# Performance work log

Hardware: AMD Instinct MI355X
Metric: run time of the kernel (lower is better)

## Reference

```python
import jax, jax.numpy as jnp
import numpy as np

N_NODES = 50000
N_EDGES = 800000
HIDDEN = 128
HEADS = 4
HEAD_DIM = HIDDEN // HEADS
LAYERS = 2


def _lin(k, fan_in, fan_out):
    # xavier_uniform with gain=0.1, stored as [in, out]
    lim = 0.1 * np.sqrt(6.0 / (fan_in + fan_out))
    return jax.random.uniform(k, (fan_in, fan_out), jnp.float32, -lim, lim)


def setup_inputs() -> dict:
    key = jax.random.key(0)
    ks = jax.random.split(key, 20)
    x = jax.random.normal(ks[0], (N_NODES, HIDDEN), jnp.float32)
    edge_index = jax.random.randint(ks[1], (2, N_EDGES), 0, N_NODES, jnp.int64)
    Wi = _lin(ks[2], HIDDEN, HIDDEN); bi = jnp.zeros((HIDDEN,), jnp.float32)
    def stack(base):
        kk = jax.random.split(jax.random.fold_in(key, base), LAYERS)
        return jnp.stack([_lin(kk[l], HIDDEN, HIDDEN) for l in range(LAYERS)])
    Wq, Wk, Wv, Wo = stack(10), stack(11), stack(12), stack(13)
    bq = jnp.zeros((LAYERS, HIDDEN), jnp.float32)
    bk = jnp.zeros((LAYERS, HIDDEN), jnp.float32)
    bv = jnp.zeros((LAYERS, HIDDEN), jnp.float32)
    bo = jnp.zeros((LAYERS, HIDDEN), jnp.float32)
    kk1 = jax.random.split(jax.random.fold_in(key, 20), LAYERS)
    kk2 = jax.random.split(jax.random.fold_in(key, 21), LAYERS)
    W1 = jnp.stack([_lin(kk1[l], HIDDEN, 2 * HIDDEN) for l in range(LAYERS)])
    b1 = jnp.zeros((LAYERS, 2 * HIDDEN), jnp.float32)
    W2 = jnp.stack([_lin(kk2[l], 2 * HIDDEN, HIDDEN) for l in range(LAYERS)])
    b2 = jnp.zeros((LAYERS, HIDDEN), jnp.float32)
    return {"x": x, "edge_index": edge_index, "Wi": Wi, "bi": bi,
            "Wq": Wq, "bq": bq, "Wk": Wk, "bk": bk, "Wv": Wv, "bv": bv,
            "Wo": Wo, "bo": bo, "W1": W1, "b1": b1, "W2": W2, "b2": b2}


def _layer(x, src, dst, Wq, bq, Wk, bk, Wv, bv, Wo, bo, W1, b1, W2, b2):
    n = x.shape[0]
    residual = x
    q = (x @ Wq + bq).reshape(n, HEADS, HEAD_DIM)
    k = (x @ Wk + bk).reshape(n, HEADS, HEAD_DIM)
    v = (x @ Wv + bv).reshape(n, HEADS, HEAD_DIM)
    q_i = q[dst]            # [E, H, D]
    k_j = k[src]            # [E, H, D]
    scale = HEAD_DIM ** -0.5
    scores = jnp.einsum('ehd,ehd->eh', q_i, k_j) * scale  # [E, H]
    # NOTE: faithful to original — softmax over ALL edges (dim=0), per head
    attn = jax.nn.softmax(scores, axis=0)
    attn_out = v[src] * attn[:, :, None]  # [E, H, D]
    agg = jax.ops.segment_sum(attn_out, dst, num_segments=n)  # [N, H, D]
    out = agg.reshape(n, HIDDEN) @ Wo + bo
    x = residual + out
    residual = x
    x = jax.nn.relu(x @ W1 + b1) @ W2 + b2
    return residual + x


def reference(x, edge_index, Wi, bi, Wq, bq, Wk, bk, Wv, bv, Wo, bo, W1, b1, W2, b2):
    src, dst = edge_index[0], edge_index[1]
    x = x @ Wi + bi
    for l in range(LAYERS):
        x = _layer(x, src, dst, Wq[l], bq[l], Wk[l], bk[l], Wv[l], bv[l],
                   Wo[l], bo[l], W1[l], b1[l], W2[l], b2[l])
    return x
```

## Files before the change

### kernel.cpp

```cpp
#include <hip/hip_runtime.h>


typedef __attribute__((ext_vector_type(8))) short bf16x8;
typedef __attribute__((ext_vector_type(4))) float f32x4;

__device__ __forceinline__ unsigned short f2bf_rne(float f) {
  unsigned int u = __builtin_bit_cast(unsigned int, f);
  u = (u + 0x7fffu + ((u >> 16) & 1u)) >> 16;
  return (unsigned short)u;
}
__device__ __forceinline__ unsigned int pack2bf(float a, float b) {
  return (unsigned int)f2bf_rne(a) | ((unsigned int)f2bf_rne(b) << 16);
}
__device__ __forceinline__ float bflo(unsigned int w) {
  return __builtin_bit_cast(float, w << 16);
}
__device__ __forceinline__ float bfhi(unsigned int w) {
  return __builtin_bit_cast(float, w & 0xffff0000u);
}

template<bool RELU, bool RES, bool OUTF, bool OUTB, bool QKVH, bool AF32>
__global__ __launch_bounds__(256)
void mgemm_k(const void* __restrict__ Ain,
             const unsigned short* __restrict__ Bt,
             const float* __restrict__ bias, const float* __restrict__ R,
             float* __restrict__ Yf, unsigned short* __restrict__ Yb,
             int M, int K, int N) {
  __shared__ __align__(16) char smem[32768];
  const int t = threadIdx.x;
  const int l = t & 63;
  const int w = t >> 6, wm = w >> 1, wn = w & 1;
  const int row0 = blockIdx.x * 64;
  const int col0 = blockIdx.y * 64;

  f32x4 acc[2][2];
#pragma unroll
  for (int m = 0; m < 2; m++)
#pragma unroll
    for (int n = 0; n < 2; n++)
#pragma unroll
      for (int r = 0; r < 4; r++) acc[m][n][r] = 0.f;

  for (int kc = 0; kc < K; kc += 128) {
    if (kc) __syncthreads();
#pragma unroll
    for (int j = 0; j < 4; j++) {
      int id = j * 256 + t;
      int row = id >> 4, c16 = id & 15;
      int gr = row0 + row; if (gr >= M) gr = M - 1;
      uint4 val;
      if (AF32) {
        const float* ap = (const float*)Ain + (size_t)gr * K + kc + c16 * 8;
        float4 f0 = *(const float4*)ap;
        float4 f1 = *(const float4*)(ap + 4);
        val.x = pack2bf(f0.x, f0.y); val.y = pack2bf(f0.z, f0.w);
        val.z = pack2bf(f1.x, f1.y); val.w = pack2bf(f1.z, f1.w);
      } else {
        val = *(const uint4*)((const unsigned short*)Ain + (size_t)gr * K + kc + c16 * 8);
      }
      *(uint4*)(smem + row * 256 + ((c16 * 16) ^ ((row & 7) << 4))) = val;
    }
#pragma unroll
    for (int j = 0; j < 4; j++) {
      int id = j * 256 + t;
      int row = id >> 4, c16 = id & 15;
      uint4 val = *(const uint4*)(Bt + (size_t)(col0 + row) * K + kc + c16 * 8);
      *(uint4*)(smem + 16384 + row * 256 + ((c16 * 16) ^ ((row & 7) << 4))) = val;
    }
    __syncthreads();

#pragma unroll
    for (int ks = 0; ks < 4; ks++) {
      const int bofs = ks * 64 + (l >> 4) * 16;
      bf16x8 a[2], b[2];
#pragma unroll
      for (int m = 0; m < 2; m++) {
        int r = wm * 32 + m * 16 + (l & 15);
        a[m] = *(const bf16x8*)(smem + r * 256 + (bofs ^ ((r & 7) << 4)));
      }
#pragma unroll
      for (int n = 0; n < 2; n++) {
        int r = wn * 32 + n * 16 + (l & 15);
        b[n] = *(const bf16x8*)(smem + 16384 + r * 256 + (bofs ^ ((r & 7) << 4)));
      }
#pragma unroll
      for (int m = 0; m < 2; m++)
#pragma unroll
        for (int n = 0; n < 2; n++)
          acc[m][n] = __builtin_amdgcn_mfma_f32_16x16x32_bf16(a[m], b[n], acc[m][n], 0, 0, 0);
    }
  }

  const int rbase = row0 + wm * 32 + ((l >> 4) << 2);
  const int cl = l & 15;
#pragma unroll
  for (int n = 0; n < 2; n++) {
    int col = col0 + wn * 32 + n * 16 + cl;
    float bb = bias[col];
#pragma unroll
    for (int m = 0; m < 2; m++) {
      int rtile = rbase + m * 16;
#pragma unroll
      for (int r = 0; r < 4; r++) {
        int row = rtile + r;
        if (row < M) {
          float o = acc[m][n][r] + bb;
          if (RES) o += R[(size_t)row * N + col];
          if (RELU) o = fmaxf(o, 0.f);
          if (OUTF) Yf[(size_t)row * N + col] = o;
          if (OUTB) {
            unsigned short vb = f2bf_rne(o);
            if (QKVH) {
              if (col < 128) {
                Yb[(size_t)row * 128 + col] = vb;
              } else if (col < 256) {
                int cc = col - 128, head = cc >> 5, dd = cc & 31;
                Yb[(size_t)M * 128 + ((size_t)head * M + row) * 32 + dd] = vb;
              } else {
                Yb[(size_t)M * 256 + (size_t)row * 128 + (col - 256)] = vb;
              }
            } else {
              Yb[(size_t)row * N + col] = vb;
            }
          }
        }
      }
    }
  }
}

__global__ __launch_bounds__(256)
void wtc_k(const float* __restrict__ src, unsigned short* __restrict__ dst,
           int K, int N, int cnt, int dstStrideM) {
  int o = blockIdx.x * 256 + threadIdx.x;
  int total = cnt * K * N;
  if (o >= total) return;
  int m = o / (K * N);
  int rem = o - m * K * N;
  int n = rem / K;
  int k = rem - n * K;
  dst[(size_t)m * dstStrideM + (size_t)n * K + k] = f2bf_rne(src[(size_t)m * K * N + (size_t)k * N + n]);
}

__global__ __launch_bounds__(256)
void bcat_k(const float* __restrict__ bq, const float* __restrict__ bk,
            const float* __restrict__ bv, float* __restrict__ bqkv) {
  int idx = blockIdx.x * 256 + threadIdx.x;
  if (idx >= 768) return;
  int l = idx / 384, c = idx - l * 384;
  float v = (c < 128) ? bq[l * 128 + c] : (c < 256) ? bk[l * 128 + c - 128] : bv[l * 128 + c - 256];
  bqkv[idx] = v;
}

__global__ __launch_bounds__(256)
void rs_hist8_k(const int* __restrict__ key, int* __restrict__ gh,
                int E, int shift, int nblk) {
  __shared__ int h[256];
  int t = threadIdx.x, b = blockIdx.x;
  h[t] = 0;
  __syncthreads();
#pragma unroll
  for (int j = 0; j < 8; j++) {
    int i = b * 2048 + j * 256 + t;
    if (i < E) atomicAdd(&h[(key[i] >> shift) & 255], 1);
  }
  __syncthreads();
  gh[t * nblk + b] = h[t];
}

__global__ __launch_bounds__(256)
void scanA_k(const int* __restrict__ a, int* __restrict__ bsum, int n) {
  __shared__ int sm[256];
  int b = blockIdx.x, t = threadIdx.x;
  int base = b * 2048 + t * 8;
  int s = 0;
#pragma unroll
  for (int j = 0; j < 8; j++) {
    int i = base + j;
    if (i < n) s += a[i];
  }
  sm[t] = s; __syncthreads();
  for (int d = 128; d >= 1; d >>= 1) {
    if (t < d) sm[t] += sm[t + d];
    __syncthreads();
  }
  if (t == 0) bsum[b] = sm[0];
}

__global__ __launch_bounds__(64)
void scanB_k(int* __restrict__ bsum, int nb) {
  if (threadIdx.x == 0 && blockIdx.x == 0) {
    int run = 0;
    for (int b = 0; b < nb; b++) { int v = bsum[b]; bsum[b] = run; run += v; }
  }
}

__global__ __launch_bounds__(256)
void scanC_k(int* __restrict__ a, const int* __restrict__ bsum, int n) {
  __shared__ int sm[256];
  int b = blockIdx.x, t = threadIdx.x;
  int base = b * 2048 + t * 8;
  int vals[8];
  int s = 0;
#pragma unroll
  for (int j = 0; j < 8; j++) {
    int i = base + j;
    vals[j] = (i < n) ? a[i] : 0;
    s += vals[j];
  }
  sm[t] = s; __syncthreads();
  for (int d = 1; d < 256; d <<= 1) {
    int v = (t >= d) ? sm[t - d] : 0;
    __syncthreads();
    sm[t] += v;
    __syncthreads();
  }
  int run = bsum[b] + sm[t] - s;
#pragma unroll
  for (int j = 0; j < 8; j++) {
    int i = base + j;
    if (i < n) { a[i] = run; run += vals[j]; }
  }
}

__global__ __launch_bounds__(256)
void rs_scatter8_k(const int* __restrict__ keyIn, const int* __restrict__ payIn,
                   int* __restrict__ keyOut, int* __restrict__ payOut,
                   const int* __restrict__ gh, int E, int shift, int nblk) {
  __shared__ int base[256];
  __shared__ int wcnt[4][256];
  int t = threadIdx.x, b = blockIdx.x;
  int w = t >> 6, ln = t & 63;
  unsigned long long lmask = (1ull << ln) - 1ull;
  base[t] = gh[t * nblk + b];
  wcnt[0][t] = 0; wcnt[1][t] = 0; wcnt[2][t] = 0; wcnt[3][t] = 0;
  __syncthreads();
  for (int j = 0; j < 8; j++) {
    int i = b * 2048 + j * 256 + t;
    bool valid = i < E;
    int kv = valid ? keyIn[i] : 0;
    int d = (kv >> shift) & 255;
    if (valid) atomicAdd(&wcnt[w][d], 1);
    unsigned long long mm = __ballot(valid);
#pragma unroll
    for (int bit = 0; bit < 8; bit++) {
      unsigned long long bb = __ballot((d >> bit) & 1);
      mm &= ((d >> bit) & 1) ? bb : ~bb;
    }
    int myrank = __popcll(mm & lmask);
    __syncthreads();
    if (valid) {
      int wbase = 0;
      for (int w2 = 0; w2 < w; w2++) wbase += wcnt[w2][d];
      int pos = base[d] + wbase + myrank;
      keyOut[pos] = kv;
      payOut[pos] = payIn ? payIn[i] : i;
    }
    __syncthreads();
    base[t] += wcnt[0][t] + wcnt[1][t] + wcnt[2][t] + wcnt[3][t];
    wcnt[0][t] = 0; wcnt[1][t] = 0; wcnt[2][t] = 0; wcnt[3][t] = 0;
    __syncthreads();
  }
}

__global__ __launch_bounds__(256)
void boundsmeta_k(const int* __restrict__ key, const int* __restrict__ pay,
                  const int* __restrict__ src, int* __restrict__ off,
                  int* __restrict__ srcP, int E, int N) {
  int i = blockIdx.x * 256 + threadIdx.x;
  if (i >= E) return;
  srcP[i] = src[pay[i]];
  int k1 = key[i];
  int k0 = (i == 0) ? -1 : key[i - 1];
  for (int d = k0 + 1; d <= k1; d++) off[d] = i;
  if (i == E - 1) {
    for (int d = k1 + 1; d <= N; d++) off[d] = E;
  }
}

__global__ __launch_bounds__(256)
void scores_k(const unsigned short* __restrict__ QKV,
              const int* __restrict__ srcP, const int* __restrict__ dstP,
              float* __restrict__ Sp, float* __restrict__ psum,
              int E, int Nn, float scale, int nb) {
  __shared__ float sm[256];
  int t = threadIdx.x, h = blockIdx.y;
  int i = blockIdx.x * 256 + t;
  float ex = 0.f;
  if (i < E) {
    const uint4* qp = (const uint4*)(QKV + (size_t)dstP[i] * 128 + h * 32);
    const uint4* kp = (const uint4*)(QKV + (size_t)Nn * 128 + ((size_t)h * Nn + srcP[i]) * 32);
    float acc = 0.f;
#pragma unroll
    for (int j = 0; j < 4; j++) {
      uint4 q4 = qp[j], k4 = kp[j];
      acc += bflo(q4.x) * bflo(k4.x) + bfhi(q4.x) * bfhi(k4.x);
      acc += bflo(q4.y) * bflo(k4.y) + bfhi(q4.y) * bfhi(k4.y);
      acc += bflo(q4.z) * bflo(k4.z) + bfhi(q4.z) * bfhi(k4.z);
      acc += bflo(q4.w) * bflo(k4.w) + bfhi(q4.w) * bfhi(k4.w);
    }
    ex = expf(acc * scale);
    Sp[(size_t)h * E + i] = ex;
  }
  sm[t] = ex; __syncthreads();
  for (int s = 128; s >= 1; s >>= 1) {
    if (t < s) sm[t] += sm[t + s];
    __syncthreads();
  }
  if (t == 0) psum[h * nb + blockIdx.x] = sm[0];
}

__global__ __launch_bounds__(256)
void reduceIz_k(const float* __restrict__ psum, float* __restrict__ iz, int nb) {
  __shared__ float sm[256];
  int h = blockIdx.x, t = threadIdx.x;
  float a = 0.f;
  for (int j = t; j < nb; j += 256) a += psum[h * nb + j];
  sm[t] = a; __syncthreads();
  for (int s = 128; s >= 1; s >>= 1) {
    if (t < s) sm[t] += sm[t + s];
    __syncthreads();
  }
  if (t == 0) iz[h] = 1.0f / sm[0];
}

__global__ __launch_bounds__(256)
void gatheragg_k(const float* __restrict__ Sp, const float* __restrict__ iz,
                 const unsigned short* __restrict__ QKV,
                 const int* __restrict__ srcP, const int* __restrict__ off,
                 unsigned short* __restrict__ AGb, int Nn, int E) {
  int node = blockIdx.x * 4 + (threadIdx.x >> 6);
  if (node >= Nn) return;
  int l = threadIdx.x & 63;
  int p = l >> 5;
  int q = l & 31;
  int h = q >> 3;
  const unsigned short* Vb = QKV + (size_t)Nn * 256 + q * 4;
  const float* Sph = Sp + (size_t)h * E;
  float izh = iz[h];
  int lo = off[node], hi = off[node + 1];
  float a0 = 0.f, a1 = 0.f, a2 = 0.f, a3 = 0.f;
  int i = lo + p;
  for (; i + 6 < hi; i += 8) {
    int s0 = srcP[i], s1 = srcP[i + 2], s2 = srcP[i + 4], s3 = srcP[i + 6];
    float c0 = Sph[i] * izh, c1 = Sph[i + 2] * izh;
    float c2 = Sph[i + 4] * izh, c3 = Sph[i + 6] * izh;
    uint2 v0 = *(const uint2*)(Vb + (size_t)s0 * 128);
    uint2 v1 = *(const uint2*)(Vb + (size_t)s1 * 128);
    uint2 v2 = *(const uint2*)(Vb + (size_t)s2 * 128);
    uint2 v3 = *(const uint2*)(Vb + (size_t)s3 * 128);
    a0 = fmaf(c0, bflo(v0.x), a0); a1 = fmaf(c0, bfhi(v0.x), a1);
    a2 = fmaf(c0, bflo(v0.y), a2); a3 = fmaf(c0, bfhi(v0.y), a3);
    a0 = fmaf(c1, bflo(v1.x), a0); a1 = fmaf(c1, bfhi(v1.x), a1);
    a2 = fmaf(c1, bflo(v1.y), a2); a3 = fmaf(c1, bfhi(v1.y), a3);
    a0 = fmaf(c2, bflo(v2.x), a0); a1 = fmaf(c2, bfhi(v2.x), a1);
    a2 = fmaf(c2, bflo(v2.y), a2); a3 = fmaf(c2, bfhi(v2.y), a3);
    a0 = fmaf(c3, bflo(v3.x), a0); a1 = fmaf(c3, bfhi(v3.x), a1);
    a2 = fmaf(c3, bflo(v3.y), a2); a3 = fmaf(c3, bfhi(v3.y), a3);
  }
  for (; i < hi; i += 2) {
    int s = srcP[i];
    float c = Sph[i] * izh;
    uint2 v = *(const uint2*)(Vb + (size_t)s * 128);
    a0 = fmaf(c, bflo(v.x), a0); a1 = fmaf(c, bfhi(v.x), a1);
    a2 = fmaf(c, bflo(v.y), a2); a3 = fmaf(c, bfhi(v.y), a3);
  }
  a0 += __shfl_down(a0, 32); a1 += __shfl_down(a1, 32);
  a2 += __shfl_down(a2, 32); a3 += __shfl_down(a3, 32);
  if (p == 0) {
    uint2 out;
    out.x = pack2bf(a0, a1);
    out.y = pack2bf(a2, a3);
    *(uint2*)(AGb + (size_t)node * 128 + q * 4) = out;
  }
}

extern "C" void kernel_launch(void* const* d_in, const int* in_sizes, int n_in,
                              void* d_out, int out_size, void* d_ws, size_t ws_size,
                              hipStream_t stream) {
  const float* x_in = (const float*)d_in[0];
  const int*   ei   = (const int*)d_in[1];
  const float* Wi = (const float*)d_in[2];
  const float* bi = (const float*)d_in[3];
  const float* Wq = (const float*)d_in[4];  const float* bq = (const float*)d_in[5];
  const float* Wk = (const float*)d_in[6];  const float* bk = (const float*)d_in[7];
  const float* Wv = (const float*)d_in[8];  const float* bv = (const float*)d_in[9];
  const float* Wo = (const float*)d_in[10]; const float* bo = (const float*)d_in[11];
  const float* W1 = (const float*)d_in[12]; const float* b1 = (const float*)d_in[13];
  const float* W2 = (const float*)d_in[14]; const float* b2 = (const float*)d_in[15];

  const int N = in_sizes[0] / 128;
  const int E = in_sizes[1] / 2;
  const int* src = ei;
  const int* dst = ei + E;

  char* w = (char*)d_ws;
  auto alloc = [&](size_t bytes) -> char* {
    char* p = w;
    w += (bytes + 255) & ~(size_t)255;
    return p;
  };
  float*          X    = (float*)alloc((size_t)N * 128 * 4);
  unsigned short* Xb   = (unsigned short*)alloc((size_t)N * 128 * 2);
  unsigned short* QKVb = (unsigned short*)alloc((size_t)N * 384 * 2);
  unsigned short* Hb   = QKVb;
  unsigned short* AGb  = (unsigned short*)alloc((size_t)N * 128 * 2);
  float*          Sp   = (float*)alloc((size_t)E * 4 * 4);
  const int nb = (E + 255) / 256;
  float* psum = (float*)alloc((size_t)4 * nb * 4);
  float* iz   = (float*)alloc(16);
  unsigned short* WiT   = (unsigned short*)alloc(16384 * 2);
  unsigned short* WqkvT = (unsigned short*)alloc((size_t)2 * 384 * 128 * 2);
  unsigned short* WoT   = (unsigned short*)alloc((size_t)2 * 16384 * 2);
  unsigned short* W1T   = (unsigned short*)alloc((size_t)2 * 32768 * 2);
  unsigned short* W2T   = (unsigned short*)alloc((size_t)2 * 32768 * 2);
  float* bqkv = (float*)alloc(768 * 4);
  int* off  = (int*)alloc((size_t)(N + 1) * 4);
  int* kA   = (int*)alloc((size_t)E * 4);
  int* pA   = (int*)alloc((size_t)E * 4);
  int* kB   = (int*)alloc((size_t)E * 4);
  int* pB   = (int*)alloc((size_t)E * 4);
  int* srcP = (int*)alloc((size_t)E * 4);
  const int nblk = (E + 2047) / 2048;
  const int ghn  = 256 * nblk;
  int* gh   = (int*)alloc((size_t)ghn * 4);
  int* bsum = (int*)alloc(256 * 4);

  const float scale = 0.17677669529663687f;
  dim3 blk(256);
  const int gx = (N + 63) / 64;
  dim3 gP(gx, 2), gQKV(gx, 6), gW1(gx, 4);
  const int gEe = (E + 255) / 256;
  const int nsb = (ghn + 2047) / 2048;
  dim3 gSc(nb, 4);
  const int gAgg = (N + 3) / 4;

  rs_hist8_k<<<nblk, blk, 0, stream>>>(dst, gh, E, 0, nblk);
  scanA_k<<<nsb, blk, 0, stream>>>(gh, bsum, ghn);
  scanB_k<<<1, 64, 0, stream>>>(bsum, nsb);
  scanC_k<<<nsb, blk, 0, stream>>>(gh, bsum, ghn);
  rs_scatter8_k<<<nblk, blk, 0, stream>>>(dst, nullptr, kA, pA, gh, E, 0, nblk);
  rs_hist8_k<<<nblk, blk, 0, stream>>>(kA, gh, E, 8, nblk);
  scanA_k<<<nsb, blk, 0, stream>>>(gh, bsum, ghn);
  scanB_k<<<1, 64, 0, stream>>>(bsum, nsb);
  scanC_k<<<nsb, blk, 0, stream>>>(gh, bsum, ghn);
  rs_scatter8_k<<<nblk, blk, 0, stream>>>(kA, pA, kB, pB, gh, E, 8, nblk);
  boundsmeta_k<<<gEe, blk, 0, stream>>>(kB, pB, src, off, srcP, E, N);
  int* dstP = kB;

  wtc_k<<<(16384 + 255) / 256, blk, 0, stream>>>(Wi, WiT, 128, 128, 1, 16384);
  wtc_k<<<(2 * 16384 + 255) / 256, blk, 0, stream>>>(Wq, WqkvT, 128, 128, 2, 384 * 128);
  wtc_k<<<(2 * 16384 + 255) / 256, blk, 0, stream>>>(Wk, WqkvT + 128 * 128, 128, 128, 2, 384 * 128);
  wtc_k<<<(2 * 16384 + 255) / 256, blk, 0, stream>>>(Wv, WqkvT + 256 * 128, 128, 128, 2, 384 * 128);
  wtc_k<<<(2 * 16384 + 255) / 256, blk, 0, stream>>>(Wo, WoT, 128, 128, 2, 16384);
  wtc_k<<<(2 * 32768 + 255) / 256, blk, 0, stream>>>(W1, W1T, 128, 256, 2, 32768);
  wtc_k<<<(2 * 32768 + 255) / 256, blk, 0, stream>>>(W2, W2T, 256, 128, 2, 32768);
  bcat_k<<<3, blk, 0, stream>>>(bq, bk, bv, bqkv);

  mgemm_k<false, false, true, true, false, true><<<gP, blk, 0, stream>>>(
      x_in, WiT, bi, nullptr, X, Xb, N, 128, 128);

  for (int l = 0; l < 2; l++) {
    const float* bo_l = bo + l * 128;
    const float* b1_l = b1 + l * 256;
    const float* b2_l = b2 + l * 128;

    mgemm_k<false, false, false, true, true, false><<<gQKV, blk, 0, stream>>>(
        Xb, WqkvT + (size_t)l * 384 * 128, bqkv + l * 384, nullptr, nullptr, QKVb, N, 128, 384);

    scores_k<<<gSc, blk, 0, stream>>>(QKVb, srcP, dstP, Sp, psum, E, N, scale, nb);
    reduceIz_k<<<4, blk, 0, stream>>>(psum, iz, nb);

    gatheragg_k<<<gAgg, blk, 0, stream>>>(Sp, iz, QKVb, srcP, off, AGb, N, E);

    mgemm_k<false, true, true, true, false, false><<<gP, blk, 0, stream>>>(
        AGb, WoT + (size_t)l * 16384, bo_l, X, X, Xb, N, 128, 128);
    mgemm_k<true, false, false, true, false, false><<<gW1, blk, 0, stream>>>(
        Xb, W1T + (size_t)l * 32768, b1_l, nullptr, nullptr, Hb, N, 128, 256);
    if (l == 0) {
      mgemm_k<false, true, true, true, false, false><<<gP, blk, 0, stream>>>(
          Hb, W2T + (size_t)l * 32768, b2_l, X, X, Xb, N, 256, 128);
    } else {
      mgemm_k<false, true, true, false, false, false><<<gP, blk, 0, stream>>>(
          Hb, W2T + (size_t)l * 32768, b2_l, X, (float*)d_out, nullptr, N, 256, 128);
    }
  }
}
```

Measured before the change: 440.7 us.

## Use row-major QKV with per-node CSR score kernel and fused scatter

```diff
diff --git a/kernel.cpp b/kernel.cpp
--- a/kernel.cpp
+++ b/kernel.cpp
@@ -18,8 +18,15 @@
 __device__ __forceinline__ float bfhi(unsigned int w) {
   return __builtin_bit_cast(float, w & 0xffff0000u);
 }
-
-template<bool RELU, bool RES, bool OUTF, bool OUTB, bool QKVH, bool AF32>
+__device__ __forceinline__ float dot8(uint4 a, uint4 b) {
+  float s = bflo(a.x) * bflo(b.x) + bfhi(a.x) * bfhi(b.x);
+  s += bflo(a.y) * bflo(b.y) + bfhi(a.y) * bfhi(b.y);
+  s += bflo(a.z) * bflo(b.z) + bfhi(a.z) * bfhi(b.z);
+  s += bflo(a.w) * bflo(b.w) + bfhi(a.w) * bfhi(b.w);
+  return s;
+}
+
+template<bool RELU, bool RES, bool OUTF, bool OUTB, bool AF32>
 __global__ __launch_bounds__(256)
 void mgemm_k(const void* __restrict__ Ain,
              const unsigned short* __restrict__ Bt,
@@ -108,21 +115,7 @@
           if (RES) o += R[(size_t)row * N + col];
           if (RELU) o = fmaxf(o, 0.f);
           if (OUTF) Yf[(size_t)row * N + col] = o;
-          if (OUTB) {
-            unsigned short vb = f2bf_rne(o);
-            if (QKVH) {
-              if (col < 128) {
-                Yb[(size_t)row * 128 + col] = vb;
-              } else if (col < 256) {
-                int cc = col - 128, head = cc >> 5, dd = cc & 31;
-                Yb[(size_t)M * 128 + ((size_t)head * M + row) * 32 + dd] = vb;
-              } else {
-                Yb[(size_t)M * 256 + (size_t)row * 128 + (col - 256)] = vb;
-              }
-            } else {
-              Yb[(size_t)row * N + col] = vb;
-            }
-          }
+          if (OUTB) Yb[(size_t)row * N + col] = f2bf_rne(o);
         }
       }
     }
@@ -153,6 +146,75 @@
 }
 
 __global__ __launch_bounds__(256)
+void zeroi_k(int* __restrict__ p, int n) {
+  int i = blockIdx.x * 256 + threadIdx.x;
+  if (i < n) p[i] = 0;
+}
+
+__global__ __launch_bounds__(256)
+void histdst_k(const int* __restrict__ dst, int* __restrict__ cnt, int E) {
+  int i = blockIdx.x * 256 + threadIdx.x;
+  if (i < E) atomicAdd(&cnt[dst[i]], 1);
+}
+
+__global__ __launch_bounds__(256)
+void scan1_k(const int* __restrict__ cnt, int* __restrict__ bsum, int N) {
+  __shared__ int sm[256];
+  int b = blockIdx.x, t = threadIdx.x;
+  int base = b * 2048 + t * 8;
+  int s = 0;
+#pragma unroll
+  for (int j = 0; j < 8; j++) {
+    int i = base + j;
+    if (i < N) s += cnt[i];
+  }
+  sm[t] = s; __syncthreads();
+  for (int d = 128; d >= 1; d >>= 1) {
+    if (t < d) sm[t] += sm[t + d];
+    __syncthreads();
+  }
+  if (t == 0) bsum[b] = sm[0];
+}
+
+__global__ __launch_bounds__(64)
+void scan2_k(int* __restrict__ bsum, int* __restrict__ off, int nb, int N) {
+  if (threadIdx.x == 0 && blockIdx.x == 0) {
+    int run = 0;
+    for (int b = 0; b < nb; b++) { int v = bsum[b]; bsum[b] = run; run += v; }
+    off[N] = run;
+  }
+}
+
+__global__ __launch_bounds__(256)
+void scan3_k(const int* __restrict__ cnt, const int* __restrict__ bsum,
+             int* __restrict__ off, int N) {
+  __shared__ int sm[256];
+  int b = blockIdx.x, t = threadIdx.x;
+  int base = b * 2048 + t * 8;
+  int vals[8];
+  int s = 0;
+#pragma unroll
+  for (int j = 0; j < 8; j++) {
+    int i = base + j;
+    vals[j] = (i < N) ? cnt[i] : 0;
+    s += vals[j];
+  }
+  sm[t] = s; __syncthreads();
+  for (int d = 1; d < 256; d <<= 1) {
+    int v = (t >= d) ? sm[t - d] : 0;
+    __syncthreads();
+    sm[t] += v;
+    __syncthreads();
+  }
+  int run = bsum[b] + sm[t] - s;
+#pragma unroll
+  for (int j = 0; j < 8; j++) {
+    int i = base + j;
+    if (i < N) { off[i] = run; run += vals[j]; }
+  }
+}
+
+__global__ __launch_bounds__(256)
 void rs_hist8_k(const int* __restrict__ key, int* __restrict__ gh,
                 int E, int shift, int nblk) {
   __shared__ int h[256];
@@ -224,7 +286,7 @@
 }
 
 __global__ __launch_bounds__(256)
-void rs_scatter8_k(const int* __restrict__ keyIn, const int* __restrict__ payIn,
+void rs_scatter8_k(const int* __restrict__ keyIn,
                    int* __restrict__ keyOut, int* __restrict__ payOut,
                    const int* __restrict__ gh, int E, int shift, int nblk) {
   __shared__ int base[256];
@@ -254,7 +316,7 @@
       for (int w2 = 0; w2 < w; w2++) wbase += wcnt[w2][d];
       int pos = base[d] + wbase + myrank;
       keyOut[pos] = kv;
-      payOut[pos] = payIn ? payIn[i] : i;
+      payOut[pos] = i;
     }
     __syncthreads();
     base[t] += wcnt[0][t] + wcnt[1][t] + wcnt[2][t] + wcnt[3][t];
@@ -264,50 +326,94 @@
 }
 
 __global__ __launch_bounds__(256)
-void boundsmeta_k(const int* __restrict__ key, const int* __restrict__ pay,
-                  const int* __restrict__ src, int* __restrict__ off,
-                  int* __restrict__ srcP, int E, int N) {
-  int i = blockIdx.x * 256 + threadIdx.x;
-  if (i >= E) return;
-  srcP[i] = src[pay[i]];
-  int k1 = key[i];
-  int k0 = (i == 0) ? -1 : key[i - 1];
-  for (int d = k0 + 1; d <= k1; d++) off[d] = i;
-  if (i == E - 1) {
-    for (int d = k1 + 1; d <= N; d++) off[d] = E;
+void rs_scatter8f_k(const int* __restrict__ keyIn, const int* __restrict__ payIn,
+                    const int* __restrict__ src, int* __restrict__ srcP,
+                    const int* __restrict__ gh, int E, int shift, int nblk) {
+  __shared__ int base[256];
+  __shared__ int wcnt[4][256];
+  int t = threadIdx.x, b = blockIdx.x;
+  int w = t >> 6, ln = t & 63;
+  unsigned long long lmask = (1ull << ln) - 1ull;
+  base[t] = gh[t * nblk + b];
+  wcnt[0][t] = 0; wcnt[1][t] = 0; wcnt[2][t] = 0; wcnt[3][t] = 0;
+  __syncthreads();
+  for (int j = 0; j < 8; j++) {
+    int i = b * 2048 + j * 256 + t;
+    bool valid = i < E;
+    int kv = valid ? keyIn[i] : 0;
+    int d = (kv >> shift) & 255;
+    int sv = valid ? src[payIn ? payIn[i] : i] : 0;
+    if (valid) atomicAdd(&wcnt[w][d], 1);
+    unsigned long long mm = __ballot(valid);
+#pragma unroll
+    for (int bit = 0; bit < 8; bit++) {
+      unsigned long long bb = __ballot((d >> bit) & 1);
+      mm &= ((d >> bit) & 1) ? bb : ~bb;
+    }
+    int myrank = __popcll(mm & lmask);
+    __syncthreads();
+    if (valid) {
+      int wbase = 0;
+      for (int w2 = 0; w2 < w; w2++) wbase += wcnt[w2][d];
+      int pos = base[d] + wbase + myrank;
+      srcP[pos] = sv;
+    }
+    __syncthreads();
+    base[t] += wcnt[0][t] + wcnt[1][t] + wcnt[2][t] + wcnt[3][t];
+    wcnt[0][t] = 0; wcnt[1][t] = 0; wcnt[2][t] = 0; wcnt[3][t] = 0;
+    __syncthreads();
   }
 }
 
 __global__ __launch_bounds__(256)
 void scores_k(const unsigned short* __restrict__ QKV,
-              const int* __restrict__ srcP, const int* __restrict__ dstP,
+              const int* __restrict__ srcP, const int* __restrict__ off,
               float* __restrict__ Sp, float* __restrict__ psum,
-              int E, int Nn, float scale, int nb) {
-  __shared__ float sm[256];
-  int t = threadIdx.x, h = blockIdx.y;
-  int i = blockIdx.x * 256 + t;
-  float ex = 0.f;
-  if (i < E) {
-    const uint4* qp = (const uint4*)(QKV + (size_t)dstP[i] * 128 + h * 32);
-    const uint4* kp = (const uint4*)(QKV + (size_t)Nn * 128 + ((size_t)h * Nn + srcP[i]) * 32);
-    float acc = 0.f;
-#pragma unroll
-    for (int j = 0; j < 4; j++) {
-      uint4 q4 = qp[j], k4 = kp[j];
-      acc += bflo(q4.x) * bflo(k4.x) + bfhi(q4.x) * bfhi(k4.x);
-      acc += bflo(q4.y) * bflo(k4.y) + bfhi(q4.y) * bfhi(k4.y);
-      acc += bflo(q4.z) * bflo(k4.z) + bfhi(q4.z) * bfhi(k4.z);
-      acc += bflo(q4.w) * bflo(k4.w) + bfhi(q4.w) * bfhi(k4.w);
-    }
-    ex = expf(acc * scale);
-    Sp[(size_t)h * E + i] = ex;
-  }
-  sm[t] = ex; __syncthreads();
-  for (int s = 128; s >= 1; s >>= 1) {
-    if (t < s) sm[t] += sm[t + s];
-    __syncthreads();
-  }
-  if (t == 0) psum[h * nb + blockIdx.x] = sm[0];
+              int Nn, float scale) {
+  __shared__ float ps[4][4];
+  int t = threadIdx.x;
+  int wv = t >> 6, l = t & 63;
+  int g = l >> 4, q = l & 15, h = q >> 2;
+  int node = blockIdx.x * 4 + wv;
+  float accp = 0.f;
+  if (node < Nn) {
+    uint4 qf = *(const uint4*)(QKV + (size_t)node * 384 + q * 8);
+    int lo = off[node], hi = off[node + 1];
+    int i = lo + g;
+    for (; i + 4 < hi; i += 8) {
+      int s0 = srcP[i], s1 = srcP[i + 4];
+      uint4 k0 = *(const uint4*)(QKV + (size_t)s0 * 384 + 128 + q * 8);
+      uint4 k1 = *(const uint4*)(QKV + (size_t)s1 * 384 + 128 + q * 8);
+      float d0 = dot8(qf, k0);
+      float d1 = dot8(qf, k1);
+      d0 += __shfl_xor(d0, 1); d0 += __shfl_xor(d0, 2);
+      d1 += __shfl_xor(d1, 1); d1 += __shfl_xor(d1, 2);
+      if ((q & 3) == 0) {
+        float e0 = expf(d0 * scale);
+        float e1 = expf(d1 * scale);
+        Sp[(size_t)i * 4 + h] = e0;
+        Sp[(size_t)(i + 4) * 4 + h] = e1;
+        accp += e0 + e1;
+      }
+    }
+    if (i < hi) {
+      int s = srcP[i];
+      uint4 kf = *(const uint4*)(QKV + (size_t)s * 384 + 128 + q * 8);
+      float d = dot8(qf, kf);
+      d += __shfl_xor(d, 1); d += __shfl_xor(d, 2);
+      if ((q & 3) == 0) {
+        float e = expf(d * scale);
+        Sp[(size_t)i * 4 + h] = e;
+        accp += e;
+      }
+    }
+  }
+  accp += __shfl_down(accp, 32);
+  accp += __shfl_down(accp, 16);
+  if (g == 0 && (q & 3) == 0) ps[wv][h] = accp;
+  __syncthreads();
+  if (t < 4) psum[(size_t)t * gridDim.x + blockIdx.x] =
+      ps[0][t] + ps[1][t] + ps[2][t] + ps[3][t];
 }
 
 __global__ __launch_bounds__(256)
@@ -315,7 +421,7 @@
   __shared__ float sm[256];
   int h = blockIdx.x, t = threadIdx.x;
   float a = 0.f;
-  for (int j = t; j < nb; j += 256) a += psum[h * nb + j];
+  for (int j = t; j < nb; j += 256) a += psum[(size_t)h * nb + j];
   sm[t] = a; __syncthreads();
   for (int s = 128; s >= 1; s >>= 1) {
     if (t < s) sm[t] += sm[t + s];
@@ -328,50 +434,54 @@
 void gatheragg_k(const float* __restrict__ Sp, const float* __restrict__ iz,
                  const unsigned short* __restrict__ QKV,
                  const int* __restrict__ srcP, const int* __restrict__ off,
-                 unsigned short* __restrict__ AGb, int Nn, int E) {
+                 unsigned short* __restrict__ AGb, int Nn) {
   int node = blockIdx.x * 4 + (threadIdx.x >> 6);
   if (node >= Nn) return;
   int l = threadIdx.x & 63;
-  int p = l >> 5;
-  int q = l & 31;
-  int h = q >> 3;
-  const unsigned short* Vb = QKV + (size_t)Nn * 256 + q * 4;
-  const float* Sph = Sp + (size_t)h * E;
+  int g = l >> 4, q = l & 15, h = q >> 2;
+  const unsigned short* Vb = QKV + 256 + q * 8;
   float izh = iz[h];
   int lo = off[node], hi = off[node + 1];
   float a0 = 0.f, a1 = 0.f, a2 = 0.f, a3 = 0.f;
-  int i = lo + p;
-  for (; i + 6 < hi; i += 8) {
-    int s0 = srcP[i], s1 = srcP[i + 2], s2 = srcP[i + 4], s3 = srcP[i + 6];
-    float c0 = Sph[i] * izh, c1 = Sph[i + 2] * izh;
-    float c2 = Sph[i + 4] * izh, c3 = Sph[i + 6] * izh;
-    uint2 v0 = *(const uint2*)(Vb + (size_t)s0 * 128);
-    uint2 v1 = *(const uint2*)(Vb + (size_t)s1 * 128);
-    uint2 v2 = *(const uint2*)(Vb + (size_t)s2 * 128);
-    uint2 v3 = *(const uint2*)(Vb + (size_t)s3 * 128);
+  float a4 = 0.f, a5 = 0.f, a6 = 0.f, a7 = 0.f;
+  int i = lo + g;
+  for (; i + 4 < hi; i += 8) {
+    int s0 = srcP[i], s1 = srcP[i + 4];
+    float c0 = Sp[(size_t)i * 4 + h] * izh;
+    float c1 = Sp[(size_t)(i + 4) * 4 + h] * izh;
+    uint4 v0 = *(const uint4*)(Vb + (size_t)s0 * 384);
+    uint4 v1 = *(const uint4*)(Vb + (size_t)s1 * 384);
     a0 = fmaf(c0, bflo(v0.x), a0); a1 = fmaf(c0, bfhi(v0.x), a1);
     a2 = fmaf(c0, bflo(v0.y), a2); a3 = fmaf(c0, bfhi(v0.y), a3);
+    a4 = fmaf(c0, bflo(v0.z), a4); a5 = fmaf(c0, bfhi(v0.z), a5);
+    a6 = fmaf(c0, bflo(v0.w), a6); a7 = fmaf(c0, bfhi(v0.w), a7);
     a0 = fmaf(c1, bflo(v1.x), a0); a1 = fmaf(c1, bfhi(v1.x), a1);
     a2 = fmaf(c1, bflo(v1.y), a2); a3 = fmaf(c1, bfhi(v1.y), a3);
-    a0 = fmaf(c2, bflo(v2.x), a0); a1 = fmaf(c2, bfhi(v2.x), a1);
-    a2 = fmaf(c2, bflo(v2.y), a2); a3 = fmaf(c2, bfhi(v2.y), a3);
-    a0 = fmaf(c3, bflo(v3.x), a0); a1 = fmaf(c3, bfhi(v3.x), a1);
-    a2 = fmaf(c3, bflo(v3.y), a2); a3 = fmaf(c3, bfhi(v3.y), a3);
-  }
-  for (; i < hi; i += 2) {
+    a4 = fmaf(c1, bflo(v1.z), a4); a5 = fmaf(c1, bfhi(v1.z), a5);
+    a6 = fmaf(c1, bflo(v1.w), a6); a7 = fmaf(c1, bfhi(v1.w), a7);
+  }
+  if (i < hi) {
     int s = srcP[i];
-    float c = Sph[i] * izh;
-    uint2 v = *(const uint2*)(Vb + (size_t)s * 128);
+    float c = Sp[(size_t)i * 4 + h] * izh;
+    uint4 v = *(const uint4*)(Vb + (size_t)s * 384);
     a0 = fmaf(c, bflo(v.x), a0); a1 = fmaf(c, bfhi(v.x), a1);
     a2 = fmaf(c, bflo(v.y), a2); a3 = fmaf(c, bfhi(v.y), a3);
-  }
-  a0 += __shfl_down(a0, 32); a1 += __shfl_down(a1, 32);
-  a2 += __shfl_down(a2, 32); a3 += __shfl_down(a3, 32);
-  if (p == 0) {
-    uint2 out;
-    out.x = pack2bf(a0, a1);
-    out.y = pack2bf(a2, a3);
-    *(uint2*)(AGb + (size_t)node * 128 + q * 4) = out;
+    a4 = fmaf(c, bflo(v.z), a4); a5 = fmaf(c, bfhi(v.z), a5);
+    a6 = fmaf(c, bflo(v.w), a6); a7 = fmaf(c, bfhi(v.w), a7);
+  }
+  a0 += __shfl_down(a0, 32); a0 += __shfl_down(a0, 16);
+  a1 += __shfl_down(a1, 32); a1 += __shfl_down(a1, 16);
+  a2 += __shfl_down(a2, 32); a2 += __shfl_down(a2, 16);
+  a3 += __shfl_down(a3, 32); a3 += __shfl_down(a3, 16);
+  a4 += __shfl_down(a4, 32); a4 += __shfl_down(a4, 16);
+  a5 += __shfl_down(a5, 32); a5 += __shfl_down(a5, 16);
+  a6 += __shfl_down(a6, 32); a6 += __shfl_down(a6, 16);
+  a7 += __shfl_down(a7, 32); a7 += __shfl_down(a7, 16);
+  if (g == 0) {
+    uint4 out;
+    out.x = pack2bf(a0, a1); out.y = pack2bf(a2, a3);
+    out.z = pack2bf(a4, a5); out.w = pack2bf(a6, a7);
+    *(uint4*)(AGb + (size_t)node * 128 + q * 8) = out;
   }
 }
 
@@ -406,8 +516,8 @@
   unsigned short* Hb   = QKVb;
   unsigned short* AGb  = (unsigned short*)alloc((size_t)N * 128 * 2);
   float*          Sp   = (float*)alloc((size_t)E * 4 * 4);
-  const int nb = (E + 255) / 256;
-  float* psum = (float*)alloc((size_t)4 * nb * 4);
+  const int nbS = (N + 3) / 4;
+  float* psum = (float*)alloc((size_t)4 * nbS * 4);
   float* iz   = (float*)alloc(16);
   unsigned short* WiT   = (unsigned short*)alloc(16384 * 2);
   unsigned short* WqkvT = (unsigned short*)alloc((size_t)2 * 384 * 128 * 2);
@@ -416,10 +526,9 @@
   unsigned short* W2T   = (unsigned short*)alloc((size_t)2 * 32768 * 2);
   float* bqkv = (float*)alloc(768 * 4);
   int* off  = (int*)alloc((size_t)(N + 1) * 4);
+  int* cnt  = (int*)alloc((size_t)N * 4);
   int* kA   = (int*)alloc((size_t)E * 4);
   int* pA   = (int*)alloc((size_t)E * 4);
-  int* kB   = (int*)alloc((size_t)E * 4);
-  int* pB   = (int*)alloc((size_t)E * 4);
   int* srcP = (int*)alloc((size_t)E * 4);
   const int nblk = (E + 2047) / 2048;
   const int ghn  = 256 * nblk;
@@ -432,21 +541,25 @@
   dim3 gP(gx, 2), gQKV(gx, 6), gW1(gx, 4);
   const int gEe = (E + 255) / 256;
   const int nsb = (ghn + 2047) / 2048;
-  dim3 gSc(nb, 4);
-  const int gAgg = (N + 3) / 4;
+  const int nsbN = (N + 2047) / 2048;
+  const int gN = (N + 255) / 256;
+
+  zeroi_k<<<gN, blk, 0, stream>>>(cnt, N);
+  histdst_k<<<gEe, blk, 0, stream>>>(dst, cnt, E);
+  scan1_k<<<nsbN, blk, 0, stream>>>(cnt, bsum, N);
+  scan2_k<<<1, 64, 0, stream>>>(bsum, off, nsbN, N);
+  scan3_k<<<nsbN, blk, 0, stream>>>(cnt, bsum, off, N);
 
   rs_hist8_k<<<nblk, blk, 0, stream>>>(dst, gh, E, 0, nblk);
   scanA_k<<<nsb, blk, 0, stream>>>(gh, bsum, ghn);
   scanB_k<<<1, 64, 0, stream>>>(bsum, nsb);
   scanC_k<<<nsb, blk, 0, stream>>>(gh, bsum, ghn);
-  rs_scatter8_k<<<nblk, blk, 0, stream>>>(dst, nullptr, kA, pA, gh, E, 0, nblk);
+  rs_scatter8_k<<<nblk, blk, 0, stream>>>(dst, kA, pA, gh, E, 0, nblk);
   rs_hist8_k<<<nblk, blk, 0, stream>>>(kA, gh, E, 8, nblk);
   scanA_k<<<nsb, blk, 0, stream>>>(gh, bsum, ghn);
   scanB_k<<<1, 64, 0, stream>>>(bsum, nsb);
   scanC_k<<<nsb, blk, 0, stream>>>(gh, bsum, ghn);
-  rs_scatter8_k<<<nblk, blk, 0, stream>>>(kA, pA, kB, pB, gh, E, 8, nblk);
-  boundsmeta_k<<<gEe, blk, 0, stream>>>(kB, pB, src, off, srcP, E, N);
-  int* dstP = kB;
+  rs_scatter8f_k<<<nblk, blk, 0, stream>>>(kA, pA, src, srcP, gh, E, 8, nblk);
 
   wtc_k<<<(16384 + 255) / 256, blk, 0, stream>>>(Wi, WiT, 128, 128, 1, 16384);
   wtc_k<<<(2 * 16384 + 255) / 256, blk, 0, stream>>>(Wq, WqkvT, 128, 128, 2, 384 * 128);
@@ -457,7 +570,7 @@
   wtc_k<<<(2 * 32768 + 255) / 256, blk, 0, stream>>>(W2, W2T, 256, 128, 2, 32768);
   bcat_k<<<3, blk, 0, stream>>>(bq, bk, bv, bqkv);
 
-  mgemm_k<false, false, true, true, false, true><<<gP, blk, 0, stream>>>(
+  mgemm_k<false, false, true, true, true><<<gP, blk, 0, stream>>>(
       x_in, WiT, bi, nullptr, X, Xb, N, 128, 128);
 
   for (int l = 0; l < 2; l++) {
@@ -465,23 +578,23 @@
     const float* b1_l = b1 + l * 256;
     const float* b2_l = b2 + l * 128;
 
-    mgemm_k<false, false, false, true, true, false><<<gQKV, blk, 0, stream>>>(
+    mgemm_k<false, false, false, true, false><<<gQKV, blk, 0, stream>>>(
         Xb, WqkvT + (size_t)l * 384 * 128, bqkv + l * 384, nullptr, nullptr, QKVb, N, 128, 384);
 
-    scores_k<<<gSc, blk, 0, stream>>>(QKVb, srcP, dstP, Sp, psum, E, N, scale, nb);
-    reduceIz_k<<<4, blk, 0, stream>>>(psum, iz, nb);
-
-    gatheragg_k<<<gAgg, blk, 0, stream>>>(Sp, iz, QKVb, srcP, off, AGb, N, E);
-
-    mgemm_k<false, true, true, true, false, false><<<gP, blk, 0, stream>>>(
+    scores_k<<<nbS, blk, 0, stream>>>(QKVb, srcP, off, Sp, psum, N, scale);
+    reduceIz_k<<<4, blk, 0, stream>>>(psum, iz, nbS);
+
+    gatheragg_k<<<nbS, blk, 0, stream>>>(Sp, iz, QKVb, srcP, off, AGb, N);
+
+    mgemm_k<false, true, true, true, false><<<gP, blk, 0, stream>>>(
         AGb, WoT + (size_t)l * 16384, bo_l, X, X, Xb, N, 128, 128);
-    mgemm_k<true, false, false, true, false, false><<<gW1, blk, 0, stream>>>(
+    mgemm_k<true, false, false, true, false><<<gW1, blk, 0, stream>>>(
         Xb, W1T + (size_t)l * 32768, b1_l, nullptr, nullptr, Hb, N, 128, 256);
     if (l == 0) {
-      mgemm_k<false, true, true, true, false, false><<<gP, blk, 0, stream>>>(
+      mgemm_k<false, true, true, true, false><<<gP, blk, 0, stream>>>(
           Hb, W2T + (size_t)l * 32768, b2_l, X, X, Xb, N, 256, 128);
     } else {
-      mgemm_k<false, true, true, false, false, false><<<gP, blk, 0, stream>>>(
+      mgemm_k<false, true, true, false, false><<<gP, blk, 0, stream>>>(
           Hb, W2T + (size_t)l * 32768, b2_l, X, (float*)d_out, nullptr, N, 256, 128);
     }
   }
```

Measured after the change: 490.9 us. 11.4% more time.
